# Optimization experiments

Hardware: AMD Instinct MI355X
Metric: run time of the kernel (lower is better)

The kernel has to match this reference:

```python
import jax, jax.numpy as jnp
import numpy as np

HEAD_SIZE = 64
N_EMB = 384
B, S = 512, 256

def setup_inputs() -> dict:
    key = jax.random.key(0)
    k1, k2, k3, k4 = jax.random.split(key, 4)
    x = jax.random.normal(k1, (B, S, N_EMB), dtype=jnp.float32)
    scale = 1.0 / np.sqrt(N_EMB)
    Wq = jax.random.normal(k2, (N_EMB, HEAD_SIZE), dtype=jnp.float32) * scale
    Wk = jax.random.normal(k3, (N_EMB, HEAD_SIZE), dtype=jnp.float32) * scale
    Wv = jax.random.normal(k4, (N_EMB, HEAD_SIZE), dtype=jnp.float32) * scale
    return {"x": x, "Wq": Wq, "Wk": Wk, "Wv": Wv}

def reference(x, Wq, Wk, Wv):
    # Projections (Linear, no bias): [B,S,E] @ [E,H] -> [B,S,H]
    q = jnp.einsum('bse,eh->bsh', x, Wq)
    k = jnp.einsum('bse,eh->bsh', x, Wk)
    v = jnp.einsum('bse,eh->bsh', x, Wv)
    # Scores: [B,S,S], scaled by 1/sqrt(head_size)
    scores = jnp.einsum('bqh,bkh->bqk', q, k) / jnp.sqrt(jnp.asarray(HEAD_SIZE, x.dtype))
    seq_len = x.shape[1]
    causal = jnp.tril(jnp.ones((seq_len, seq_len), dtype=bool))
    scores = jnp.where(causal[None, :, :], scores, jnp.asarray(-jnp.inf, scores.dtype))
    attn = jax.nn.softmax(scores, axis=-1)
    # dropout_ratio=0 -> identity
    out = jnp.einsum('bqk,bkh->bqh', attn, v)
    return out
```

## Files before the change

kernel.cpp:

```cpp
#include <hip/hip_runtime.h>
#include <hip/hip_bf16.h>


#define NB   512
#define SS   256
#define EE   384
#define HH   64

typedef short bf16x8 __attribute__((ext_vector_type(8)));
typedef float f32x4  __attribute__((ext_vector_type(4)));

__device__ __forceinline__ short f2bf(float f) {
  union { float f; unsigned u; } x; x.f = f;
  unsigned r = x.u + 0x7fffu + ((x.u >> 16) & 1u);
  return (short)(r >> 16);
}

__global__ __launch_bounds__(256) void prep_w_kernel(
    const float* __restrict__ Wq, const float* __restrict__ Wk,
    const float* __restrict__ Wv, short* __restrict__ wfrag) {
  int t = blockIdx.x * 256 + threadIdx.x;
  if (t >= 12 * 12 * 64) return;
  int ks  = t / (12 * 64);
  int rem = t % (12 * 64);
  int nf  = rem / 64;
  int l   = rem % 64;
  int l15 = l & 15, lhi = l >> 4;
  int ncat = nf * 16 + l15;
  const float* W = (ncat < 64) ? Wq : (ncat < 128 ? Wk : Wv);
  int n = ncat & 63;
  short* dst = wfrag + (size_t)t * 8;
#pragma unroll
  for (int j = 0; j < 8; ++j) {
    int kk = ks * 32 + lhi * 8 + j;
    dst[j] = f2bf(W[kk * 64 + n]);
  }
}

__global__ __launch_bounds__(256, 2) void fused_kernel(
    const float* __restrict__ x, const short* __restrict__ wfrag,
    float* __restrict__ out) {
  __shared__ __align__(16) short Kl[SS * HH];
  __shared__ __align__(16) short Vt[HH * SS];
  __shared__ __align__(16) short xst[16 * EE];
  __shared__ __align__(16) short ring[2 * 16 * 64];

  int b    = blockIdx.x;
  int tid  = threadIdx.x;
  int lane = tid & 63, wv = tid >> 6;
  int l15  = lane & 15, lhi = lane >> 4;
  int sw   = l15 & 7;
  const float* xb = x + (size_t)b * SS * EE;

  bf16x8 af[12][3];
#pragma unroll
  for (int ks = 0; ks < 12; ++ks)
#pragma unroll
    for (int h = 0; h < 3; ++h)
      af[ks][h] = *(const bf16x8*)(wfrag + ((size_t)(ks * 12 + wv * 3 + h) * 64 + lane) * 8);

  f32x4 st[6];
  auto loadch = [&](int ch) {
    const float* p0 = xb + (size_t)ch * 16 * EE;
#pragma unroll
    for (int i = 0; i < 3; ++i) {
      const f32x4* p = (const f32x4*)(p0 + (size_t)(tid + 256 * i) * 8);
      st[2 * i]     = p[0];
      st[2 * i + 1] = p[1];
    }
  };
  auto writech = [&]() {
#pragma unroll
    for (int i = 0; i < 3; ++i) {
      int c = tid + 256 * i;
      int row = c / 48, cg = c % 48;
      union { bf16x8 vv; __hip_bfloat162 h2[4]; } u;
      u.h2[0] = __float22bfloat162_rn(make_float2(st[2*i][0],   st[2*i][1]));
      u.h2[1] = __float22bfloat162_rn(make_float2(st[2*i][2],   st[2*i][3]));
      u.h2[2] = __float22bfloat162_rn(make_float2(st[2*i+1][0], st[2*i+1][1]));
      u.h2[3] = __float22bfloat162_rn(make_float2(st[2*i+1][2], st[2*i+1][3]));
      *(bf16x8*)(xst + row * 384 + ((cg ^ (row & 7)) * 8)) = u.vv;
    }
  };

  bf16x8 qa[4][2];

  loadch(0);
  writech();
  for (int ch = 0; ch < 16; ++ch) {
    __syncthreads();

    if (ch >= 1) {
      int rtp = ch - 1;
      const short* slot = ring + (rtp & 1) * 1024;
#pragma unroll
      for (int uu = 0; uu < 4; ++uu) {
        int rtu = (uu == 0) ? wv : (uu == 1) ? (7 - wv) : (uu == 2) ? (8 + wv) : (15 - wv);
        if (rtp == rtu) {
#pragma unroll
          for (int kf = 0; kf < 2; ++kf)
            qa[uu][kf] = *(const bf16x8*)(slot + l15 * 64 + ((kf * 32 + lhi * 8) ^ (sw << 3)));
        }
      }
    }

    if (ch < 15) loadch(ch + 1);

    f32x4 acc[3];
#pragma unroll
    for (int h = 0; h < 3; ++h) acc[h] = (f32x4){0.f, 0.f, 0.f, 0.f};
#pragma unroll
    for (int ks = 0; ks < 12; ++ks) {
      bf16x8 bx = *(const bf16x8*)(xst + l15 * 384 + (((ks * 4 + lhi) ^ sw) * 8));
#pragma unroll
      for (int h = 0; h < 3; ++h)
        acc[h] = __builtin_amdgcn_mfma_f32_16x16x32_bf16(af[ks][h], bx, acc[h], 0, 0, 0);
    }

    int row  = ch * 16 + l15;
    int srow = ((row & 8) >> 1) | (row & 3);
#pragma unroll
    for (int ht = 0; ht < 3; ++ht) {
      int f = wv * 3 + ht;
      int ncat = f * 16 + lhi * 4;
      if (f < 8) {
        union { short4 s4; __hip_bfloat162 h2[2]; } o;
        o.h2[0] = __float22bfloat162_rn(make_float2(acc[ht][0], acc[ht][1]));
        o.h2[1] = __float22bfloat162_rn(make_float2(acc[ht][2], acc[ht][3]));
        if (f < 4) {
          *(short4*)(ring + (ch & 1) * 1024 + l15 * 64 + (ncat ^ (sw << 3))) = o.s4;
        } else {
          int col = ncat - 64;
          *(short4*)(Kl + row * 64 + (col ^ (srow << 3))) = o.s4;
        }
      } else {
#pragma unroll
        for (int j = 0; j < 4; ++j) {
          int h = ncat - 128 + j;
          Vt[h * 256 + (row ^ ((h & 7) << 3))] = f2bf(acc[ht][j]);
        }
      }
    }
    __syncthreads();
    if (ch < 15) writech();
  }
  __syncthreads();
  {
    const short* slot = ring + 1024;
#pragma unroll
    for (int uu = 0; uu < 4; ++uu) {
      int rtu = (uu == 0) ? wv : (uu == 1) ? (7 - wv) : (uu == 2) ? (8 + wv) : (15 - wv);
      if (rtu == 15) {
#pragma unroll
        for (int kf = 0; kf < 2; ++kf)
          qa[uu][kf] = *(const bf16x8*)(slot + l15 * 64 + ((kf * 32 + lhi * 8) ^ (sw << 3)));
      }
    }
  }

  size_t obase = (size_t)b * SS * HH;
#pragma unroll
  for (int u = 0; u < 4; ++u) {
    int rt = (u == 0) ? wv : (u == 1) ? (7 - wv) : (u == 2) ? (8 + wv) : (15 - wv);
    int qrow0 = rt * 16;
    int twp = (rt + 2) & ~1;
    int nk  = twp >> 1;
    int qg  = qrow0 + l15;

    float mx = -3.0e38f;
    for (int t = 0; t < twp; ++t) {
      int kc = (t >> 1) * 32 + ((l15 >> 2) << 3) + ((t & 1) << 2) + (l15 & 3);
      const short* kp = Kl + kc * 64;
      bf16x8 kb0 = *(const bf16x8*)(kp + ((lhi * 8) ^ (sw << 3)));
      bf16x8 kb1 = *(const bf16x8*)(kp + ((32 + lhi * 8) ^ (sw << 3)));
      f32x4 a = (f32x4){0.f, 0.f, 0.f, 0.f};
      a = __builtin_amdgcn_mfma_f32_16x16x32_bf16(kb0, qa[u][0], a, 0, 0, 0);
      a = __builtin_amdgcn_mfma_f32_16x16x32_bf16(kb1, qa[u][1], a, 0, 0, 0);
#pragma unroll
      for (int r = 0; r < 4; ++r) {
        int kg = (t >> 1) * 32 + lhi * 8 + ((t & 1) << 2) + r;
        float v = a[r] * 0.125f;
        mx = (kg <= qg) ? fmaxf(mx, v) : mx;
      }
    }
    mx = fmaxf(mx, __shfl_xor(mx, 16));
    mx = fmaxf(mx, __shfl_xor(mx, 32));

    float sm = 0.f;
    f32x4 o[4];
#pragma unroll
    for (int nf = 0; nf < 4; ++nf) o[nf] = (f32x4){0.f, 0.f, 0.f, 0.f};
    for (int kc2 = 0; kc2 < nk; ++kc2) {
      int kcA = kc2 * 32 + ((l15 >> 2) << 3) + (l15 & 3);
      const short* kpA = Kl + kcA * 64;
      const short* kpB = kpA + 4 * 64;
      bf16x8 a0 = *(const bf16x8*)(kpA + ((lhi * 8) ^ (sw << 3)));
      bf16x8 a1 = *(const bf16x8*)(kpA + ((32 + lhi * 8) ^ (sw << 3)));
      bf16x8 b0 = *(const bf16x8*)(kpB + ((lhi * 8) ^ (sw << 3)));
      bf16x8 b1 = *(const bf16x8*)(kpB + ((32 + lhi * 8) ^ (sw << 3)));
      f32x4 aA = (f32x4){0.f, 0.f, 0.f, 0.f};
      aA = __builtin_amdgcn_mfma_f32_16x16x32_bf16(a0, qa[u][0], aA, 0, 0, 0);
      aA = __builtin_amdgcn_mfma_f32_16x16x32_bf16(a1, qa[u][1], aA, 0, 0, 0);
      f32x4 aB = (f32x4){0.f, 0.f, 0.f, 0.f};
      aB = __builtin_amdgcn_mfma_f32_16x16x32_bf16(b0, qa[u][0], aB, 0, 0, 0);
      aB = __builtin_amdgcn_mfma_f32_16x16x32_bf16(b1, qa[u][1], aB, 0, 0, 0);
      float pA[4], pB[4];
#pragma unroll
      for (int r = 0; r < 4; ++r) {
        int kgA = kc2 * 32 + lhi * 8 + r;
        pA[r] = (kgA <= qg) ? __expf(aA[r] * 0.125f - mx) : 0.f;
        pB[r] = (kgA + 4 <= qg) ? __expf(aB[r] * 0.125f - mx) : 0.f;
        sm += pA[r] + pB[r];
      }
      union { bf16x8 v; __hip_bfloat162 h2[4]; } pu;
      pu.h2[0] = __float22bfloat162_rn(make_float2(pA[0], pA[1]));
      pu.h2[1] = __float22bfloat162_rn(make_float2(pA[2], pA[3]));
      pu.h2[2] = __float22bfloat162_rn(make_float2(pB[0], pB[1]));
      pu.h2[3] = __float22bfloat162_rn(make_float2(pB[2], pB[3]));
      int kofs = kc2 * 32 + lhi * 8;
#pragma unroll
      for (int nf = 0; nf < 4; ++nf) {
        int hrow = nf * 16 + l15;
        bf16x8 vb = *(const bf16x8*)(Vt + hrow * 256 + (kofs ^ ((hrow & 7) << 3)));
        o[nf] = __builtin_amdgcn_mfma_f32_16x16x32_bf16(pu.v, vb, o[nf], 0, 0, 0);
      }
    }
    sm += __shfl_xor(sm, 16);
    sm += __shfl_xor(sm, 32);
    float inv = 1.f / sm;
    float invq[4];
#pragma unroll
    for (int r = 0; r < 4; ++r) invq[r] = __shfl(inv, lhi * 4 + r);

#pragma unroll
    for (int nf = 0; nf < 4; ++nf)
#pragma unroll
      for (int r = 0; r < 4; ++r) {
        int q = qrow0 + lhi * 4 + r;
        int h = nf * 16 + l15;
        out[obase + (size_t)q * HH + h] = o[nf][r] * invq[r];
      }
  }
}

extern "C" void kernel_launch(void* const* d_in, const int* in_sizes, int n_in,
                              void* d_out, int out_size, void* d_ws, size_t ws_size,
                              hipStream_t stream) {
  const float* x  = (const float*)d_in[0];
  const float* Wq = (const float*)d_in[1];
  const float* Wk = (const float*)d_in[2];
  const float* Wv = (const float*)d_in[3];
  float* out = (float*)d_out;

  short* wfrag = (short*)d_ws;

  prep_w_kernel<<<36, 256, 0, stream>>>(Wq, Wk, Wv, wfrag);
  fused_kernel<<<512, 256, 0, stream>>>(x, wfrag, out);
}
```

Measured before the change: 67.07 us.

## Use six waves per block, spill Q to global, and cache scores in registers

Raises the block from 4 to 6 waves so each wave computes two 16-column projection tiles instead of three, cutting per-wave weight registers and MFMA work per chunk. Q is now written as bf16 to a global workspace instead of passing through an LDS ring, and each wave reads its Q rows back before attention. Attention keeps all QK scores in a 16-entry register array, so K is read and the QK MFMAs are issued once instead of twice for max and sum. Row tiles are rebalanced across 6 waves with uneven counts. The register-held scores may raise register pressure and limit the requested 3 blocks per CU, and the Q round trip adds global traffic.

```diff
diff --git a/kernel.cpp b/kernel.cpp
--- a/kernel.cpp
+++ b/kernel.cpp
@@ -37,13 +37,12 @@
   }
 }
 
-__global__ __launch_bounds__(256, 2) void fused_kernel(
+__global__ __launch_bounds__(384, 3) void fused_kernel(
     const float* __restrict__ x, const short* __restrict__ wfrag,
-    float* __restrict__ out) {
+    short* __restrict__ qws, float* __restrict__ out) {
   __shared__ __align__(16) short Kl[SS * HH];
   __shared__ __align__(16) short Vt[HH * SS];
   __shared__ __align__(16) short xst[16 * EE];
-  __shared__ __align__(16) short ring[2 * 16 * 64];
 
   int b    = blockIdx.x;
   int tid  = threadIdx.x;
@@ -51,88 +50,67 @@
   int l15  = lane & 15, lhi = lane >> 4;
   int sw   = l15 & 7;
   const float* xb = x + (size_t)b * SS * EE;
-
-  bf16x8 af[12][3];
+  short* qbb = qws + (size_t)b * SS * HH;
+
+  bf16x8 af[12][2];
 #pragma unroll
   for (int ks = 0; ks < 12; ++ks)
 #pragma unroll
-    for (int h = 0; h < 3; ++h)
-      af[ks][h] = *(const bf16x8*)(wfrag + ((size_t)(ks * 12 + wv * 3 + h) * 64 + lane) * 8);
-
-  f32x4 st[6];
+    for (int ht = 0; ht < 2; ++ht)
+      af[ks][ht] = *(const bf16x8*)(wfrag + ((size_t)(ks * 12 + wv * 2 + ht) * 64 + lane) * 8);
+
+  f32x4 st[4];
   auto loadch = [&](int ch) {
     const float* p0 = xb + (size_t)ch * 16 * EE;
 #pragma unroll
-    for (int i = 0; i < 3; ++i) {
-      const f32x4* p = (const f32x4*)(p0 + (size_t)(tid + 256 * i) * 8);
-      st[2 * i]     = p[0];
-      st[2 * i + 1] = p[1];
-    }
+    for (int i = 0; i < 4; ++i)
+      st[i] = *(const f32x4*)(p0 + (size_t)(tid + 384 * i) * 4);
   };
   auto writech = [&]() {
 #pragma unroll
-    for (int i = 0; i < 3; ++i) {
-      int c = tid + 256 * i;
-      int row = c / 48, cg = c % 48;
-      union { bf16x8 vv; __hip_bfloat162 h2[4]; } u;
-      u.h2[0] = __float22bfloat162_rn(make_float2(st[2*i][0],   st[2*i][1]));
-      u.h2[1] = __float22bfloat162_rn(make_float2(st[2*i][2],   st[2*i][3]));
-      u.h2[2] = __float22bfloat162_rn(make_float2(st[2*i+1][0], st[2*i+1][1]));
-      u.h2[3] = __float22bfloat162_rn(make_float2(st[2*i+1][2], st[2*i+1][3]));
-      *(bf16x8*)(xst + row * 384 + ((cg ^ (row & 7)) * 8)) = u.vv;
+    for (int i = 0; i < 4; ++i) {
+      int c16 = tid + 384 * i;
+      int row = c16 / 96, cg4 = c16 % 96;
+      union { short4 s4; __hip_bfloat162 h2[2]; } u;
+      u.h2[0] = __float22bfloat162_rn(make_float2(st[i][0], st[i][1]));
+      u.h2[1] = __float22bfloat162_rn(make_float2(st[i][2], st[i][3]));
+      *(short4*)(xst + row * 384 + (((cg4 >> 1) ^ (row & 7)) * 8 + (cg4 & 1) * 4)) = u.s4;
     }
   };
-
-  bf16x8 qa[4][2];
 
   loadch(0);
   writech();
   for (int ch = 0; ch < 16; ++ch) {
     __syncthreads();
-
-    if (ch >= 1) {
-      int rtp = ch - 1;
-      const short* slot = ring + (rtp & 1) * 1024;
-#pragma unroll
-      for (int uu = 0; uu < 4; ++uu) {
-        int rtu = (uu == 0) ? wv : (uu == 1) ? (7 - wv) : (uu == 2) ? (8 + wv) : (15 - wv);
-        if (rtp == rtu) {
-#pragma unroll
-          for (int kf = 0; kf < 2; ++kf)
-            qa[uu][kf] = *(const bf16x8*)(slot + l15 * 64 + ((kf * 32 + lhi * 8) ^ (sw << 3)));
-        }
-      }
-    }
-
     if (ch < 15) loadch(ch + 1);
 
-    f32x4 acc[3];
-#pragma unroll
-    for (int h = 0; h < 3; ++h) acc[h] = (f32x4){0.f, 0.f, 0.f, 0.f};
+    f32x4 acc[2];
+    acc[0] = (f32x4){0.f, 0.f, 0.f, 0.f};
+    acc[1] = (f32x4){0.f, 0.f, 0.f, 0.f};
 #pragma unroll
     for (int ks = 0; ks < 12; ++ks) {
       bf16x8 bx = *(const bf16x8*)(xst + l15 * 384 + (((ks * 4 + lhi) ^ sw) * 8));
-#pragma unroll
-      for (int h = 0; h < 3; ++h)
-        acc[h] = __builtin_amdgcn_mfma_f32_16x16x32_bf16(af[ks][h], bx, acc[h], 0, 0, 0);
+      acc[0] = __builtin_amdgcn_mfma_f32_16x16x32_bf16(af[ks][0], bx, acc[0], 0, 0, 0);
+      acc[1] = __builtin_amdgcn_mfma_f32_16x16x32_bf16(af[ks][1], bx, acc[1], 0, 0, 0);
     }
 
     int row  = ch * 16 + l15;
     int srow = ((row & 8) >> 1) | (row & 3);
 #pragma unroll
-    for (int ht = 0; ht < 3; ++ht) {
-      int f = wv * 3 + ht;
+    for (int ht = 0; ht < 2; ++ht) {
+      int f = wv * 2 + ht;
       int ncat = f * 16 + lhi * 4;
-      if (f < 8) {
-        union { short4 s4; __hip_bfloat162 h2[2]; } o;
-        o.h2[0] = __float22bfloat162_rn(make_float2(acc[ht][0], acc[ht][1]));
-        o.h2[1] = __float22bfloat162_rn(make_float2(acc[ht][2], acc[ht][3]));
-        if (f < 4) {
-          *(short4*)(ring + (ch & 1) * 1024 + l15 * 64 + (ncat ^ (sw << 3))) = o.s4;
-        } else {
-          int col = ncat - 64;
-          *(short4*)(Kl + row * 64 + (col ^ (srow << 3))) = o.s4;
-        }
+      if (f < 4) {
+        union { short4 s4; __hip_bfloat162 h2[2]; } oq;
+        oq.h2[0] = __float22bfloat162_rn(make_float2(acc[ht][0], acc[ht][1]));
+        oq.h2[1] = __float22bfloat162_rn(make_float2(acc[ht][2], acc[ht][3]));
+        *(short4*)(qbb + (size_t)row * HH + ncat) = oq.s4;
+      } else if (f < 8) {
+        int col = ncat - 64;
+        union { short4 s4; __hip_bfloat162 h2[2]; } ok;
+        ok.h2[0] = __float22bfloat162_rn(make_float2(acc[ht][0], acc[ht][1]));
+        ok.h2[1] = __float22bfloat162_rn(make_float2(acc[ht][2], acc[ht][3]));
+        *(short4*)(Kl + row * 64 + (col ^ (srow << 3))) = ok.s4;
       } else {
 #pragma unroll
         for (int j = 0; j < 4; ++j) {
@@ -145,78 +123,81 @@
     if (ch < 15) writech();
   }
   __syncthreads();
-  {
-    const short* slot = ring + 1024;
-#pragma unroll
-    for (int uu = 0; uu < 4; ++uu) {
-      int rtu = (uu == 0) ? wv : (uu == 1) ? (7 - wv) : (uu == 2) ? (8 + wv) : (15 - wv);
-      if (rtu == 15) {
-#pragma unroll
-        for (int kf = 0; kf < 2; ++kf)
-          qa[uu][kf] = *(const bf16x8*)(slot + l15 * 64 + ((kf * 32 + lhi * 8) ^ (sw << 3)));
-      }
-    }
-  }
 
   size_t obase = (size_t)b * SS * HH;
 #pragma unroll
-  for (int u = 0; u < 4; ++u) {
-    int rt = (u == 0) ? wv : (u == 1) ? (7 - wv) : (u == 2) ? (8 + wv) : (15 - wv);
+  for (int u = 0; u < 3; ++u) {
+    if (u == 2 && wv >= 4) continue;
+    int rt;
+    if (u == 0)      rt = (wv < 4) ? (13 - wv) : (19 - wv);
+    else if (u == 1) rt = (wv < 2) ? (5 - wv) : ((wv < 4) ? (6 + wv) : (2 + wv));
+    else             rt = (wv < 2) ? (2 + wv) : (wv - 2);
+
     int qrow0 = rt * 16;
-    int twp = (rt + 2) & ~1;
-    int nk  = twp >> 1;
-    int qg  = qrow0 + l15;
-
-    float mx = -3.0e38f;
-    for (int t = 0; t < twp; ++t) {
+    int twp   = (rt + 2) & ~1;
+    int nk    = twp >> 1;
+    int qg    = qrow0 + l15;
+
+    const short* qrow = qbb + (size_t)(qrow0 + l15) * HH;
+    bf16x8 qa0 = *(const bf16x8*)(qrow + lhi * 8);
+    bf16x8 qa1 = *(const bf16x8*)(qrow + 32 + lhi * 8);
+
+    f32x4 s[16];
+#pragma unroll
+    for (int t = 0; t < 16; ++t) {
+      if (t >= twp) continue;
       int kc = (t >> 1) * 32 + ((l15 >> 2) << 3) + ((t & 1) << 2) + (l15 & 3);
       const short* kp = Kl + kc * 64;
       bf16x8 kb0 = *(const bf16x8*)(kp + ((lhi * 8) ^ (sw << 3)));
       bf16x8 kb1 = *(const bf16x8*)(kp + ((32 + lhi * 8) ^ (sw << 3)));
       f32x4 a = (f32x4){0.f, 0.f, 0.f, 0.f};
-      a = __builtin_amdgcn_mfma_f32_16x16x32_bf16(kb0, qa[u][0], a, 0, 0, 0);
-      a = __builtin_amdgcn_mfma_f32_16x16x32_bf16(kb1, qa[u][1], a, 0, 0, 0);
+      a = __builtin_amdgcn_mfma_f32_16x16x32_bf16(kb0, qa0, a, 0, 0, 0);
+      a = __builtin_amdgcn_mfma_f32_16x16x32_bf16(kb1, qa1, a, 0, 0, 0);
 #pragma unroll
       for (int r = 0; r < 4; ++r) {
         int kg = (t >> 1) * 32 + lhi * 8 + ((t & 1) << 2) + r;
-        float v = a[r] * 0.125f;
-        mx = (kg <= qg) ? fmaxf(mx, v) : mx;
-      }
+        s[t][r] = (kg <= qg) ? a[r] * 0.125f : -INFINITY;
+      }
+    }
+
+    float mx = -3.0e38f;
+#pragma unroll
+    for (int t = 0; t < 16; ++t) {
+      if (t >= twp) continue;
+#pragma unroll
+      for (int r = 0; r < 4; ++r) mx = fmaxf(mx, s[t][r]);
     }
     mx = fmaxf(mx, __shfl_xor(mx, 16));
     mx = fmaxf(mx, __shfl_xor(mx, 32));
-
     float sm = 0.f;
+#pragma unroll
+    for (int t = 0; t < 16; ++t) {
+      if (t >= twp) continue;
+#pragma unroll
+      for (int r = 0; r < 4; ++r) {
+        float p = __expf(s[t][r] - mx);
+        s[t][r] = p;
+        sm += p;
+      }
+    }
+    sm += __shfl_xor(sm, 16);
+    sm += __shfl_xor(sm, 32);
+    float inv = 1.f / sm;
+    float invq[4];
+#pragma unroll
+    for (int r = 0; r < 4; ++r) invq[r] = __shfl(inv, lhi * 4 + r);
+
     f32x4 o[4];
 #pragma unroll
     for (int nf = 0; nf < 4; ++nf) o[nf] = (f32x4){0.f, 0.f, 0.f, 0.f};
-    for (int kc2 = 0; kc2 < nk; ++kc2) {
-      int kcA = kc2 * 32 + ((l15 >> 2) << 3) + (l15 & 3);
-      const short* kpA = Kl + kcA * 64;
-      const short* kpB = kpA + 4 * 64;
-      bf16x8 a0 = *(const bf16x8*)(kpA + ((lhi * 8) ^ (sw << 3)));
-      bf16x8 a1 = *(const bf16x8*)(kpA + ((32 + lhi * 8) ^ (sw << 3)));
-      bf16x8 b0 = *(const bf16x8*)(kpB + ((lhi * 8) ^ (sw << 3)));
-      bf16x8 b1 = *(const bf16x8*)(kpB + ((32 + lhi * 8) ^ (sw << 3)));
-      f32x4 aA = (f32x4){0.f, 0.f, 0.f, 0.f};
-      aA = __builtin_amdgcn_mfma_f32_16x16x32_bf16(a0, qa[u][0], aA, 0, 0, 0);
-      aA = __builtin_amdgcn_mfma_f32_16x16x32_bf16(a1, qa[u][1], aA, 0, 0, 0);
-      f32x4 aB = (f32x4){0.f, 0.f, 0.f, 0.f};
-      aB = __builtin_amdgcn_mfma_f32_16x16x32_bf16(b0, qa[u][0], aB, 0, 0, 0);
-      aB = __builtin_amdgcn_mfma_f32_16x16x32_bf16(b1, qa[u][1], aB, 0, 0, 0);
-      float pA[4], pB[4];
-#pragma unroll
-      for (int r = 0; r < 4; ++r) {
-        int kgA = kc2 * 32 + lhi * 8 + r;
-        pA[r] = (kgA <= qg) ? __expf(aA[r] * 0.125f - mx) : 0.f;
-        pB[r] = (kgA + 4 <= qg) ? __expf(aB[r] * 0.125f - mx) : 0.f;
-        sm += pA[r] + pB[r];
-      }
+#pragma unroll
+    for (int kc2 = 0; kc2 < 8; ++kc2) {
+      if (kc2 >= nk) continue;
       union { bf16x8 v; __hip_bfloat162 h2[4]; } pu;
-      pu.h2[0] = __float22bfloat162_rn(make_float2(pA[0], pA[1]));
-      pu.h2[1] = __float22bfloat162_rn(make_float2(pA[2], pA[3]));
-      pu.h2[2] = __float22bfloat162_rn(make_float2(pB[0], pB[1]));
-      pu.h2[3] = __float22bfloat162_rn(make_float2(pB[2], pB[3]));
+      pu.h2[0] = __float22bfloat162_rn(make_float2(s[2*kc2][0],   s[2*kc2][1]));
+      pu.h2[1] = __float22bfloat162_rn(make_float2(s[2*kc2][2],   s[2*kc2][3]));
+      pu.h2[2] = __float22bfloat162_rn(make_float2(s[2*kc2+1][0], s[2*kc2+1][1]));
+      pu.h2[3] = __float22bfloat162_rn(make_float2(s[2*kc2+1][2], s[2*kc2+1][3]));
       int kofs = kc2 * 32 + lhi * 8;
 #pragma unroll
       for (int nf = 0; nf < 4; ++nf) {
@@ -225,12 +206,6 @@
         o[nf] = __builtin_amdgcn_mfma_f32_16x16x32_bf16(pu.v, vb, o[nf], 0, 0, 0);
       }
     }
-    sm += __shfl_xor(sm, 16);
-    sm += __shfl_xor(sm, 32);
-    float inv = 1.f / sm;
-    float invq[4];
-#pragma unroll
-    for (int r = 0; r < 4; ++r) invq[r] = __shfl(inv, lhi * 4 + r);
 
 #pragma unroll
     for (int nf = 0; nf < 4; ++nf)
@@ -252,8 +227,10 @@
   const float* Wv = (const float*)d_in[3];
   float* out = (float*)d_out;
 
-  short* wfrag = (short*)d_ws;
+  char* ws = (char*)d_ws;
+  short* wfrag = (short*)ws;
+  short* qws   = (short*)(ws + 262144);
 
   prep_w_kernel<<<36, 256, 0, stream>>>(Wq, Wk, Wv, wfrag);
-  fused_kernel<<<512, 256, 0, stream>>>(x, wfrag, out);
-}
+  fused_kernel<<<512, 384, 0, stream>>>(x, wfrag, qws, out);
+}
```

New measurement: 68.10 us. No clear change (+1.5%).
